# Optimization experiments

Hardware: AMD Instinct MI355X
Metric: run time of the kernel (lower is better)

## Reference

```python
import jax, jax.numpy as jnp
import numpy as np

NUM_ROUTING = 3


def squash(s, axis=-1):
    # squash(s) = |s|^2/(1+|s|^2) * s/|s|  (no epsilon, matching the torch code)
    sq = jnp.sum(s * s, axis=axis, keepdims=True)
    return sq / (1.0 + sq) * (s / jnp.sqrt(sq))


def setup_inputs() -> dict:
    key = jax.random.key(0)
    k1, k2 = jax.random.split(key)
    B, in_dim, in_num = 256, 8, 1152
    out_num, out_dim = 10, 16
    x = jax.random.normal(k1, (B, in_dim, in_num), dtype=jnp.float32)
    W = jax.random.normal(k2, (in_num, out_num, out_dim, in_dim), dtype=jnp.float32)
    return {"x": x, "W": W}


def reference(x, W):
    # x: [B, in_dim, in_num]; W: [in_num(i), out_num(j), out_dim(d), in_dim(c)]
    B = x.shape[0]
    in_num, out_num = W.shape[0], W.shape[1]
    # u_hat[i,j,b,d] = sum_c W[i,j,d,c] * x[b,c,i]
    u_hat = jnp.einsum('ijdc,bci->ijbd', W, x)
    b_ij = jnp.zeros((in_num, out_num), dtype=x.dtype)
    v = None
    for _ in range(NUM_ROUTING):
        # DGL reduce: softmax over the output-capsule axis (bucket dim)
        c = jax.nn.softmax(b_ij, axis=1)                    # [i, j]
        s = jnp.einsum('ij,ijbd->jbd', c, u_hat)            # [j, B, d]
        v = squash(s, axis=2)                               # [j, B, d]
        # edge update: b_ij += mean_b sum_d v[j,b,d] * u_hat[i,j,b,d]
        b_ij = b_ij + jnp.einsum('jbd,ijbd->ij', v, u_hat) / B
    # output: [B, out_num, out_dim, 1]
    return jnp.transpose(v, (1, 0, 2))[..., None]
```

## Files before the change

### kernel.cpp

```cpp
#include <hip/hip_runtime.h>

#define IN_NUM 1152
#define OUT_NUM 10
#define OUT_DIM 16
#define IN_DIM 8
#define NB 256
#define KTOT 9216

#define OFF_SPART 0
#define SZ_SPART (96 * OUT_NUM * OUT_DIM * NB)
#define OFF_BP (OFF_SPART + SZ_SPART)
#define SZ_BP (32 * IN_NUM * OUT_NUM)
#define OFF_VT (OFF_BP + SZ_BP)
#define SZ_VT (NB * OUT_NUM * OUT_DIM)
#define OFF_WT (OFF_VT + SZ_VT)
#define SZ_WT (OUT_NUM * OUT_DIM * KTOT)
#define OFF_WT2 (OFF_WT + SZ_WT)
#define SZ_WT2 (OUT_NUM * KTOT * OUT_DIM)
#define OFF_XT (OFF_WT2 + SZ_WT2)
#define SZ_XT (KTOT * NB)

__global__ __launch_bounds__(256) void k_prep(const float* __restrict__ x,
                                              const float* __restrict__ W,
                                              float* __restrict__ xT,
                                              float* __restrict__ Wt,
                                              float* __restrict__ Wt2) {
    __shared__ float smem[64 * 68];
    int u = blockIdx.x, t = threadIdx.x;
    if (u < 576) {
        float (*lds)[68] = (float (*)[68])smem;
        int kt = u % 144, bt = u / 144;
        int k0 = kt * 64, b0 = bt * 64;
        int r = t >> 4, c4 = (t & 15) * 4;
#pragma unroll
        for (int p = 0; p < 4; ++p) {
            int bb = p * 16 + r;
            float4 v = *reinterpret_cast<const float4*>(&x[(size_t)(b0 + bb) * KTOT + k0 + c4]);
            lds[bb][c4 + 0] = v.x; lds[bb][c4 + 1] = v.y;
            lds[bb][c4 + 2] = v.z; lds[bb][c4 + 3] = v.w;
        }
        __syncthreads();
#pragma unroll
        for (int p = 0; p < 4; ++p) {
            int kk = p * 16 + r;
            float4 o;
            o.x = lds[c4 + 0][kk]; o.y = lds[c4 + 1][kk];
            o.z = lds[c4 + 2][kk]; o.w = lds[c4 + 3][kk];
            *reinterpret_cast<float4*>(&xT[(size_t)(k0 + kk) * NB + b0 + c4]) = o;
        }
    } else {
        float (*lds2)[129] = (float (*)[129])smem;
        int w = u - 576;
        int itile = w / 10, j = w - itile * 10;
        int i0 = itile * 32;
        int r0 = t >> 5, c4b = t & 31;
#pragma unroll
        for (int rr = 0; rr < 4; ++rr) {
            int rrow = rr * 8 + r0;
            float4 w4 = *reinterpret_cast<const float4*>(
                &W[(size_t)(i0 + rrow) * 1280 + j * 128 + c4b * 4]);
            lds2[rrow][c4b * 4 + 0] = w4.x; lds2[rrow][c4b * 4 + 1] = w4.y;
            lds2[rrow][c4b * 4 + 2] = w4.z; lds2[rrow][c4b * 4 + 3] = w4.w;
        }
        __syncthreads();
        int ii = t & 31, dcq = t >> 5;
#pragma unroll
        for (int rr = 0; rr < 16; ++rr) {
            int dc = rr * 8 + dcq;
            Wt[(size_t)(j * 128 + dc) * IN_NUM + i0 + ii] = lds2[ii][dc];
        }
        int d4 = t & 3, ii2 = (t >> 2) & 31, ch0 = t >> 7;
#pragma unroll
        for (int c2 = 0; c2 < 4; ++c2) {
            int c = c2 * 2 + ch0;
            float4 o;
            o.x = lds2[ii2][(d4 * 4 + 0) * 8 + c];
            o.y = lds2[ii2][(d4 * 4 + 1) * 8 + c];
            o.z = lds2[ii2][(d4 * 4 + 2) * 8 + c];
            o.w = lds2[ii2][(d4 * 4 + 3) * 8 + c];
            *reinterpret_cast<float4*>(
                &Wt2[((size_t)j * KTOT + c * IN_NUM + i0 + ii2) * OUT_DIM + d4 * 4]) = o;
        }
    }
}

__global__ __launch_bounds__(256, 4) void k_p1(const float* __restrict__ xT,
                                               const float* __restrict__ Wt2,
                                               const float* __restrict__ bp,
                                               float* __restrict__ spart, int it) {
    __shared__ float ldc[96];
    int w = blockIdx.x, t = threadIdx.x;
    int g8 = w / 80, r = w - g8 * 80;
    int j = r >> 3, isp = g8 * 8 + (r & 7);
    int cch = isp / 12;
    int i0 = (isp - cch * 12) * 96;
    int k0 = isp * 96;
    if (t < 96) {
        float cv;
        if (it == 0) {
            cv = 0.1f;
        } else {
            int i = i0 + t;
            float bt_[OUT_NUM];
#pragma unroll
            for (int jp = 0; jp < OUT_NUM; ++jp) bt_[jp] = 0.f;
#pragma unroll 4
            for (int row = 0; row < 32; ++row) {
                const float2* p2 = reinterpret_cast<const float2*>(
                    &bp[(size_t)row * (IN_NUM * OUT_NUM) + i * OUT_NUM]);
#pragma unroll
                for (int q = 0; q < 5; ++q) {
                    float2 v = p2[q];
                    bt_[q * 2] += v.x; bt_[q * 2 + 1] += v.y;
                }
            }
            float m = -1e30f;
#pragma unroll
            for (int jp = 0; jp < OUT_NUM; ++jp) { bt_[jp] *= (1.f / NB); m = fmaxf(m, bt_[jp]); }
            float s = 0.f;
#pragma unroll
            for (int jp = 0; jp < OUT_NUM; ++jp) { bt_[jp] = __expf(bt_[jp] - m); s += bt_[jp]; }
            cv = bt_[j] / s;
        }
        ldc[t] = cv;
    }
    __syncthreads();
    const float* xp = xT + (size_t)k0 * NB + t;
    const float* wp = Wt2 + ((size_t)j * KTOT + k0) * OUT_DIM;
    float acc[16];
#pragma unroll
    for (int d = 0; d < 16; ++d) acc[d] = 0.f;
#pragma unroll 4
    for (int kk = 0; kk < 96; ++kk) {
        float xv = xp[(size_t)kk * NB];
        float xs = xv * ldc[kk];
        const float* a = wp + kk * OUT_DIM;
#pragma unroll
        for (int d = 0; d < 16; ++d) acc[d] += a[d] * xs;
    }
    float* sp = spart + ((size_t)isp * OUT_NUM + j) * (OUT_DIM * NB) + t;
#pragma unroll
    for (int d = 0; d < 16; ++d) sp[d * NB] = acc[d];
}

__global__ __launch_bounds__(256, 4) void k_p2(const float* __restrict__ spart,
                                               float* __restrict__ dst) {
    __shared__ float smem[4672];
    float (*red)[32][17] = (float (*)[32][17])smem;
    float (*nrm)[9] = (float (*)[9])(smem + 4352);
    float* cf = smem + 4640;
    int wvar = blockIdx.x, t = threadIdx.x;
    int j = wvar >> 3, bt2 = wvar & 7;
    int ie = t >> 5, bb = t & 31;
    int b = bt2 * 32 + bb;
    float acc[16];
#pragma unroll
    for (int d = 0; d < 16; ++d) acc[d] = 0.f;
    for (int q = 0; q < 12; ++q) {
        int isp = ie * 12 + q;
        const float* sp = spart + (size_t)(isp * OUT_NUM + j) * (OUT_DIM * NB) + b;
#pragma unroll
        for (int d = 0; d < 16; ++d) acc[d] += sp[d * NB];
    }
#pragma unroll
    for (int d = 0; d < 16; ++d) red[ie][bb][d] = acc[d];
    __syncthreads();
    int bb2 = t >> 3, dp = t & 7;
    float s0 = 0.f, s1 = 0.f;
#pragma unroll
    for (int e = 0; e < 8; ++e) { s0 += red[e][bb2][dp * 2]; s1 += red[e][bb2][dp * 2 + 1]; }
    nrm[bb2][dp] = s0 * s0 + s1 * s1;
    __syncthreads();
    if (t < 32) {
        float qn = 0.f;
#pragma unroll
        for (int d = 0; d < 8; ++d) qn += nrm[t][d];
        cf[t] = qn / ((1.f + qn) * sqrtf(qn));
    }
    __syncthreads();
    float cs = cf[bb2];
    float* o = dst + (size_t)(bt2 * 32 + bb2) * (OUT_NUM * OUT_DIM) + j * OUT_DIM + dp * 2;
    o[0] = s0 * cs;
    o[1] = s1 * cs;
}

__global__ __launch_bounds__(256) void k_p3(const float* __restrict__ x,
                                            const float* __restrict__ vt,
                                            const float* __restrict__ Wt,
                                            float* __restrict__ bp, int it) {
    int u = blockIdx.x, t = threadIdx.x;
    int kt = u % 36;
    int jq = u / 36;
    int j = jq >> 2, bq = jq & 3;
    int k = kt * 256 + t;
    int c = k / IN_NUM, i = k - c * IN_NUM;
    const float* xk = x + k + (size_t)(bq * 64) * KTOT;
    const float* vjb = vt + (size_t)(bq * 64) * (OUT_NUM * OUT_DIM) + j * OUT_DIM;
    float macc[16];
#pragma unroll
    for (int d = 0; d < 16; ++d) macc[d] = 0.f;
#pragma unroll 8
    for (int b = 0; b < 64; ++b) {
        float xv = xk[(size_t)b * KTOT];
        const float* vb = vjb + (size_t)b * (OUT_NUM * OUT_DIM);
#pragma unroll
        for (int d = 0; d < 16; ++d) macc[d] += vb[d] * xv;
    }
    float bs = 0.f;
#pragma unroll
    for (int d = 0; d < 16; ++d)
        bs += macc[d] * Wt[(size_t)(j * OUT_DIM + d) * KTOT + k];
    size_t idx = (size_t)(bq * 8 + c) * (IN_NUM * OUT_NUM) + (size_t)i * OUT_NUM + j;
    float prev = (it == 0) ? 0.f : bp[idx];
    bp[idx] = prev + bs;
}

extern "C" void kernel_launch(void* const* d_in, const int* in_sizes, int n_in,
                              void* d_out, int out_size, void* d_ws, size_t ws_size,
                              hipStream_t stream) {
    const float* x = (const float*)d_in[0];
    const float* W = (const float*)d_in[1];
    float* out = (float*)d_out;
    float* ws = (float*)d_ws;

    float* spart = ws + OFF_SPART;
    float* bp    = ws + OFF_BP;
    float* vt    = ws + OFF_VT;
    float* Wt    = ws + OFF_WT;
    float* Wt2   = ws + OFF_WT2;
    float* xT    = ws + OFF_XT;

    k_prep<<<dim3(936), dim3(256), 0, stream>>>(x, W, xT, Wt, Wt2);
    for (int it = 0; it < 3; ++it) {
        k_p1<<<dim3(960), dim3(256), 0, stream>>>(xT, Wt2, bp, spart, it);
        k_p2<<<dim3(80), dim3(256), 0, stream>>>(spart, it == 2 ? out : vt);
        if (it < 2) k_p3<<<dim3(1440), dim3(256), 0, stream>>>(x, vt, Wt, bp, it);
    }
}
```

Before: 122.1 us.

## Stage v in LDS and compute two k per thread in routing-logit kernel

The agreement kernel k_p3 now loads the 64x16 slice of v for its batch quarter and output capsule into shared memory once, then reads it as float4 rows. Each thread handles two adjacent k positions with float2 loads of x and Wt, so every v read is reused twice. The grid is remapped to 960 blocks of 192 threads with an interleaved block-to-tile order. This is meant to cut redundant global/L1 traffic for v and raise arithmetic per load, at the cost of more registers (32 accumulators) and a smaller block.

```diff
diff --git a/kernel.cpp b/kernel.cpp
--- a/kernel.cpp
+++ b/kernel.cpp
@@ -184,35 +184,56 @@
     o[1] = s1 * cs;
 }
 
-__global__ __launch_bounds__(256) void k_p3(const float* __restrict__ x,
+__global__ __launch_bounds__(192) void k_p3(const float* __restrict__ x,
                                             const float* __restrict__ vt,
                                             const float* __restrict__ Wt,
                                             float* __restrict__ bp, int it) {
-    int u = blockIdx.x, t = threadIdx.x;
-    int kt = u % 36;
-    int jq = u / 36;
+    __shared__ float vs[64][16];
+    int bid = blockIdx.x, t = threadIdx.x;
+    int e = bid & 7, r = bid >> 3;
+    int kt = e * 3 + (r % 3);
+    int jq = r / 3;
     int j = jq >> 2, bq = jq & 3;
-    int k = kt * 256 + t;
-    int c = k / IN_NUM, i = k - c * IN_NUM;
-    const float* xk = x + k + (size_t)(bq * 64) * KTOT;
-    const float* vjb = vt + (size_t)(bq * 64) * (OUT_NUM * OUT_DIM) + j * OUT_DIM;
-    float macc[16];
-#pragma unroll
-    for (int d = 0; d < 16; ++d) macc[d] = 0.f;
-#pragma unroll 8
+    for (int idx = t; idx < 1024; idx += 192) {
+        int b = idx >> 4, d = idx & 15;
+        vs[b][d] = vt[(size_t)(bq * 64 + b) * (OUT_NUM * OUT_DIM) + j * OUT_DIM + d];
+    }
+    __syncthreads();
+    int k0 = kt * 384 + t * 2;
+    const float* xk = x + (size_t)(bq * 64) * KTOT + k0;
+    float m0[16], m1[16];
+#pragma unroll
+    for (int d = 0; d < 16; ++d) { m0[d] = 0.f; m1[d] = 0.f; }
+#pragma unroll 4
     for (int b = 0; b < 64; ++b) {
-        float xv = xk[(size_t)b * KTOT];
-        const float* vb = vjb + (size_t)b * (OUT_NUM * OUT_DIM);
-#pragma unroll
-        for (int d = 0; d < 16; ++d) macc[d] += vb[d] * xv;
-    }
-    float bs = 0.f;
-#pragma unroll
-    for (int d = 0; d < 16; ++d)
-        bs += macc[d] * Wt[(size_t)(j * OUT_DIM + d) * KTOT + k];
-    size_t idx = (size_t)(bq * 8 + c) * (IN_NUM * OUT_NUM) + (size_t)i * OUT_NUM + j;
-    float prev = (it == 0) ? 0.f : bp[idx];
-    bp[idx] = prev + bs;
+        float2 xv = *reinterpret_cast<const float2*>(&xk[(size_t)b * KTOT]);
+        const float4* vrow = reinterpret_cast<const float4*>(vs[b]);
+        float4 v0 = vrow[0], v1 = vrow[1], v2 = vrow[2], v3 = vrow[3];
+        m0[0] += v0.x * xv.x; m0[1] += v0.y * xv.x; m0[2] += v0.z * xv.x; m0[3] += v0.w * xv.x;
+        m0[4] += v1.x * xv.x; m0[5] += v1.y * xv.x; m0[6] += v1.z * xv.x; m0[7] += v1.w * xv.x;
+        m0[8] += v2.x * xv.x; m0[9] += v2.y * xv.x; m0[10] += v2.z * xv.x; m0[11] += v2.w * xv.x;
+        m0[12] += v3.x * xv.x; m0[13] += v3.y * xv.x; m0[14] += v3.z * xv.x; m0[15] += v3.w * xv.x;
+        m1[0] += v0.x * xv.y; m1[1] += v0.y * xv.y; m1[2] += v0.z * xv.y; m1[3] += v0.w * xv.y;
+        m1[4] += v1.x * xv.y; m1[5] += v1.y * xv.y; m1[6] += v1.z * xv.y; m1[7] += v1.w * xv.y;
+        m1[8] += v2.x * xv.y; m1[9] += v2.y * xv.y; m1[10] += v2.z * xv.y; m1[11] += v2.w * xv.y;
+        m1[12] += v3.x * xv.y; m1[13] += v3.y * xv.y; m1[14] += v3.z * xv.y; m1[15] += v3.w * xv.y;
+    }
+    float bs0 = 0.f, bs1 = 0.f;
+#pragma unroll
+    for (int d = 0; d < 16; ++d) {
+        float2 w2 = *reinterpret_cast<const float2*>(&Wt[(size_t)(j * OUT_DIM + d) * KTOT + k0]);
+        bs0 += m0[d] * w2.x;
+        bs1 += m1[d] * w2.y;
+    }
+    int c = k0 / IN_NUM, i = k0 - c * IN_NUM;
+    size_t idx0 = (size_t)(bq * 8 + c) * (IN_NUM * OUT_NUM) + (size_t)i * OUT_NUM + j;
+    if (it == 0) {
+        bp[idx0] = bs0;
+        bp[idx0 + OUT_NUM] = bs1;
+    } else {
+        bp[idx0] += bs0;
+        bp[idx0 + OUT_NUM] += bs1;
+    }
 }
 
 extern "C" void kernel_launch(void* const* d_in, const int* in_sizes, int n_in,
@@ -234,6 +255,6 @@
     for (int it = 0; it < 3; ++it) {
         k_p1<<<dim3(960), dim3(256), 0, stream>>>(xT, Wt2, bp, spart, it);
         k_p2<<<dim3(80), dim3(256), 0, stream>>>(spart, it == 2 ? out : vt);
-        if (it < 2) k_p3<<<dim3(1440), dim3(256), 0, stream>>>(x, vt, Wt, bp, it);
-    }
-}
+        if (it < 2) k_p3<<<dim3(960), dim3(192), 0, stream>>>(x, vt, Wt, bp, it);
+    }
+}
```

After: 127.4 us. +4.4%, slower.

## Use bf16 MFMA for routing s-accumulation and drop x transpose

Applied to the files above, without the earlier changes.

Rewrites the per-iteration s computation in k_p1 as bf16 16x16x32 MFMA ops. The routing-weighted W slice is converted to bf16 in LDS, and x is read directly in its original layout and converted on the fly. This removes the x transpose from the prep kernel and the scalar FMA loop. The trade is lower precision (bf16 inputs with fp32 accumulation) in exchange for matrix-core throughput.

```diff
diff --git a/kernel.cpp b/kernel.cpp
--- a/kernel.cpp
+++ b/kernel.cpp
@@ -17,78 +17,59 @@
 #define SZ_WT (OUT_NUM * OUT_DIM * KTOT)
 #define OFF_WT2 (OFF_WT + SZ_WT)
 #define SZ_WT2 (OUT_NUM * KTOT * OUT_DIM)
-#define OFF_XT (OFF_WT2 + SZ_WT2)
-#define SZ_XT (KTOT * NB)
-
-__global__ __launch_bounds__(256) void k_prep(const float* __restrict__ x,
-                                              const float* __restrict__ W,
-                                              float* __restrict__ xT,
+
+typedef short bf16x8 __attribute__((ext_vector_type(8)));
+typedef float f32x4 __attribute__((ext_vector_type(4)));
+
+__device__ __forceinline__ unsigned short f2bf(float f) {
+    unsigned u = __float_as_uint(f);
+    u = (u + 0x7FFFu + ((u >> 16) & 1u)) >> 16;
+    return (unsigned short)u;
+}
+
+__global__ __launch_bounds__(256) void k_prep(const float* __restrict__ W,
                                               float* __restrict__ Wt,
                                               float* __restrict__ Wt2) {
-    __shared__ float smem[64 * 68];
+    __shared__ float lds2[32][129];
     int u = blockIdx.x, t = threadIdx.x;
-    if (u < 576) {
-        float (*lds)[68] = (float (*)[68])smem;
-        int kt = u % 144, bt = u / 144;
-        int k0 = kt * 64, b0 = bt * 64;
-        int r = t >> 4, c4 = (t & 15) * 4;
-#pragma unroll
-        for (int p = 0; p < 4; ++p) {
-            int bb = p * 16 + r;
-            float4 v = *reinterpret_cast<const float4*>(&x[(size_t)(b0 + bb) * KTOT + k0 + c4]);
-            lds[bb][c4 + 0] = v.x; lds[bb][c4 + 1] = v.y;
-            lds[bb][c4 + 2] = v.z; lds[bb][c4 + 3] = v.w;
-        }
-        __syncthreads();
-#pragma unroll
-        for (int p = 0; p < 4; ++p) {
-            int kk = p * 16 + r;
-            float4 o;
-            o.x = lds[c4 + 0][kk]; o.y = lds[c4 + 1][kk];
-            o.z = lds[c4 + 2][kk]; o.w = lds[c4 + 3][kk];
-            *reinterpret_cast<float4*>(&xT[(size_t)(k0 + kk) * NB + b0 + c4]) = o;
-        }
-    } else {
-        float (*lds2)[129] = (float (*)[129])smem;
-        int w = u - 576;
-        int itile = w / 10, j = w - itile * 10;
-        int i0 = itile * 32;
-        int r0 = t >> 5, c4b = t & 31;
-#pragma unroll
-        for (int rr = 0; rr < 4; ++rr) {
-            int rrow = rr * 8 + r0;
-            float4 w4 = *reinterpret_cast<const float4*>(
-                &W[(size_t)(i0 + rrow) * 1280 + j * 128 + c4b * 4]);
-            lds2[rrow][c4b * 4 + 0] = w4.x; lds2[rrow][c4b * 4 + 1] = w4.y;
-            lds2[rrow][c4b * 4 + 2] = w4.z; lds2[rrow][c4b * 4 + 3] = w4.w;
-        }
-        __syncthreads();
-        int ii = t & 31, dcq = t >> 5;
-#pragma unroll
-        for (int rr = 0; rr < 16; ++rr) {
-            int dc = rr * 8 + dcq;
-            Wt[(size_t)(j * 128 + dc) * IN_NUM + i0 + ii] = lds2[ii][dc];
-        }
-        int d4 = t & 3, ii2 = (t >> 2) & 31, ch0 = t >> 7;
-#pragma unroll
-        for (int c2 = 0; c2 < 4; ++c2) {
-            int c = c2 * 2 + ch0;
-            float4 o;
-            o.x = lds2[ii2][(d4 * 4 + 0) * 8 + c];
-            o.y = lds2[ii2][(d4 * 4 + 1) * 8 + c];
-            o.z = lds2[ii2][(d4 * 4 + 2) * 8 + c];
-            o.w = lds2[ii2][(d4 * 4 + 3) * 8 + c];
-            *reinterpret_cast<float4*>(
-                &Wt2[((size_t)j * KTOT + c * IN_NUM + i0 + ii2) * OUT_DIM + d4 * 4]) = o;
-        }
-    }
-}
-
-__global__ __launch_bounds__(256, 4) void k_p1(const float* __restrict__ xT,
+    int itile = u / 10, j = u - itile * 10;
+    int i0 = itile * 32;
+    int r0 = t >> 5, c4b = t & 31;
+#pragma unroll
+    for (int rr = 0; rr < 4; ++rr) {
+        int rrow = rr * 8 + r0;
+        float4 w4 = *reinterpret_cast<const float4*>(
+            &W[(size_t)(i0 + rrow) * 1280 + j * 128 + c4b * 4]);
+        lds2[rrow][c4b * 4 + 0] = w4.x; lds2[rrow][c4b * 4 + 1] = w4.y;
+        lds2[rrow][c4b * 4 + 2] = w4.z; lds2[rrow][c4b * 4 + 3] = w4.w;
+    }
+    __syncthreads();
+    int ii = t & 31, dcq = t >> 5;
+#pragma unroll
+    for (int rr = 0; rr < 16; ++rr) {
+        int dc = rr * 8 + dcq;
+        Wt[(size_t)(j * 128 + dc) * IN_NUM + i0 + ii] = lds2[ii][dc];
+    }
+    int d4 = t & 3, ii2 = (t >> 2) & 31, ch0 = t >> 7;
+#pragma unroll
+    for (int c2 = 0; c2 < 4; ++c2) {
+        int c = c2 * 2 + ch0;
+        float4 o;
+        o.x = lds2[ii2][(d4 * 4 + 0) * 8 + c];
+        o.y = lds2[ii2][(d4 * 4 + 1) * 8 + c];
+        o.z = lds2[ii2][(d4 * 4 + 2) * 8 + c];
+        o.w = lds2[ii2][(d4 * 4 + 3) * 8 + c];
+        *reinterpret_cast<float4*>(
+            &Wt2[((size_t)j * KTOT + c * IN_NUM + i0 + ii2) * OUT_DIM + d4 * 4]) = o;
+    }
+}
+
+__global__ __launch_bounds__(256, 4) void k_p1(const float* __restrict__ x,
                                                const float* __restrict__ Wt2,
                                                const float* __restrict__ bp,
                                                float* __restrict__ spart, int it) {
     __shared__ float ldc[96];
+    __shared__ unsigned short atT[16][100];
     int w = blockIdx.x, t = threadIdx.x;
     int g8 = w / 80, r = w - g8 * 80;
     int j = r >> 3, isp = g8 * 8 + (r & 7);
@@ -125,22 +106,44 @@
         ldc[t] = cv;
     }
     __syncthreads();
-    const float* xp = xT + (size_t)k0 * NB + t;
-    const float* wp = Wt2 + ((size_t)j * KTOT + k0) * OUT_DIM;
-    float acc[16];
-#pragma unroll
-    for (int d = 0; d < 16; ++d) acc[d] = 0.f;
-#pragma unroll 4
-    for (int kk = 0; kk < 96; ++kk) {
-        float xv = xp[(size_t)kk * NB];
-        float xs = xv * ldc[kk];
-        const float* a = wp + kk * OUT_DIM;
-#pragma unroll
-        for (int d = 0; d < 16; ++d) acc[d] += a[d] * xs;
-    }
-    float* sp = spart + ((size_t)isp * OUT_NUM + j) * (OUT_DIM * NB) + t;
-#pragma unroll
-    for (int d = 0; d < 16; ++d) sp[d * NB] = acc[d];
+    for (int e = t; e < 1536; e += 256) {
+        int d = e & 15, kk = e >> 4;
+        atT[d][kk] = f2bf(ldc[kk] * Wt2[((size_t)j * KTOT + k0 + kk) * OUT_DIM + d]);
+    }
+    __syncthreads();
+    int lane = t & 63, wv = t >> 6;
+    int lg = lane >> 4, lm = lane & 15;
+    bf16x8 bfr[3];
+#pragma unroll
+    for (int ks = 0; ks < 3; ++ks) {
+        const unsigned short* p0 = &atT[lm][ks * 32 + lg * 4];
+        ushort4 u0 = *reinterpret_cast<const ushort4*>(p0);
+        ushort4 u1 = *reinterpret_cast<const ushort4*>(p0 + 16);
+        bfr[ks][0] = (short)u0.x; bfr[ks][1] = (short)u0.y;
+        bfr[ks][2] = (short)u0.z; bfr[ks][3] = (short)u0.w;
+        bfr[ks][4] = (short)u1.x; bfr[ks][5] = (short)u1.y;
+        bfr[ks][6] = (short)u1.z; bfr[ks][7] = (short)u1.w;
+    }
+    float* sp = spart + ((size_t)isp * OUT_NUM + j) * (OUT_DIM * NB);
+#pragma unroll
+    for (int tb = 0; tb < 4; ++tb) {
+        int tbase = (wv * 4 + tb) * 16;
+        const float* xr = x + (size_t)(tbase + lm) * KTOT + k0 + lg * 4;
+        f32x4 acc = {0.f, 0.f, 0.f, 0.f};
+#pragma unroll
+        for (int ks = 0; ks < 3; ++ks) {
+            float4 a0 = *reinterpret_cast<const float4*>(xr + ks * 32);
+            float4 a1 = *reinterpret_cast<const float4*>(xr + ks * 32 + 16);
+            bf16x8 af;
+            af[0] = (short)f2bf(a0.x); af[1] = (short)f2bf(a0.y);
+            af[2] = (short)f2bf(a0.z); af[3] = (short)f2bf(a0.w);
+            af[4] = (short)f2bf(a1.x); af[5] = (short)f2bf(a1.y);
+            af[6] = (short)f2bf(a1.z); af[7] = (short)f2bf(a1.w);
+            acc = __builtin_amdgcn_mfma_f32_16x16x32_bf16(af, bfr[ks], acc, 0, 0, 0);
+        }
+        *reinterpret_cast<float4*>(&sp[(size_t)lm * NB + tbase + lg * 4]) =
+            make_float4(acc[0], acc[1], acc[2], acc[3]);
+    }
 }
 
 __global__ __launch_bounds__(256, 4) void k_p2(const float* __restrict__ spart,
@@ -228,11 +231,10 @@
     float* vt    = ws + OFF_VT;
     float* Wt    = ws + OFF_WT;
     float* Wt2   = ws + OFF_WT2;
-    float* xT    = ws + OFF_XT;
-
-    k_prep<<<dim3(936), dim3(256), 0, stream>>>(x, W, xT, Wt, Wt2);
+
+    k_prep<<<dim3(360), dim3(256), 0, stream>>>(W, Wt, Wt2);
     for (int it = 0; it < 3; ++it) {
-        k_p1<<<dim3(960), dim3(256), 0, stream>>>(xT, Wt2, bp, spart, it);
+        k_p1<<<dim3(960), dim3(256), 0, stream>>>(x, Wt2, bp, spart, it);
         k_p2<<<dim3(80), dim3(256), 0, stream>>>(spart, it == 2 ? out : vt);
         if (it < 2) k_p3<<<dim3(1440), dim3(256), 0, stream>>>(x, vt, Wt, bp, it);
     }
```

Measured after the change: 121.0 us. About the same (-0.8%).
